# Kernel optimization log

Hardware: AMD Instinct MI355X
Metric: run time of the kernel (lower is better)

Reference implementation:

```python
import jax, jax.numpy as jnp
import numpy as np

N_LEAVES = 32768
DEPTH = 16               # tree levels, leaves at level 0
N_NODES = 2 * N_LEAVES - 1
H = 256                  # h_size
X = 300                  # x_size
FEAT = 1024              # image feature_size
R = 49                   # image regions
VOCAB = 30000
CLASSES = 5


def setup_inputs() -> dict:
    ks = jax.random.split(jax.random.key(0), 10)
    wordid = jax.random.randint(ks[0], (N_NODES,), 0, VOCAB, dtype=jnp.int32)
    # leaves carry word tokens (mask=1), internal nodes don't (mask=0)
    mask = jnp.concatenate([jnp.ones(N_LEAVES, jnp.int32),
                            jnp.zeros(N_NODES - N_LEAVES, jnp.int32)])
    image = jax.random.normal(ks[1], (R, FEAT), dtype=jnp.float32)
    h0 = jnp.zeros((N_NODES, H), jnp.float32)
    c0 = jnp.zeros((N_NODES, H), jnp.float32)
    s = lambda k, shp, fan: jax.random.normal(k, shp, dtype=jnp.float32) * (1.0 / np.sqrt(fan))
    emb = s(ks[2], (VOCAB, X), X)
    attn_w_in = s(ks[3], (X, FEAT), FEAT)            # Attention.linear_in (no bias)
    attn_w_out = s(ks[4], (X, X + FEAT), X + FEAT)   # Attention.linear_out
    attn_b_out = jnp.zeros((X,), jnp.float32)
    w_iou = s(ks[5], (3 * H, X), X)                  # cell.W_iou (no bias)
    u_iou = s(ks[6], (3 * H, 2 * H), 2 * H)          # cell.U_iou (no bias)
    b_iou = jnp.zeros((1, 3 * H), jnp.float32)
    u_f_w = s(ks[7], (2 * H, 2 * H), 2 * H)          # cell.U_f
    u_f_b = jnp.zeros((2 * H,), jnp.float32)
    lin_w = s(ks[8], (CLASSES, H), H)                # final classifier
    lin_b = jnp.zeros((CLASSES,), jnp.float32)
    return dict(wordid=wordid, mask=mask, image=image, h0=h0, c0=c0, emb=emb,
                attn_w_in=attn_w_in, attn_w_out=attn_w_out, attn_b_out=attn_b_out,
                w_iou=w_iou, u_iou=u_iou, b_iou=b_iou, u_f_w=u_f_w, u_f_b=u_f_b,
                lin_w=lin_w, lin_b=lin_b)


def _forward(wordid, mask, image, h0, c0, emb, attn_w_in, attn_w_out, attn_b_out,
             w_iou, u_iou, b_iou, u_f_w, u_f_b, lin_w, lin_b):
    # --- embedding + attention over image regions ---
    embeds = emb[wordid * mask]                                  # [N, X]
    img_in = image @ attn_w_in.T                                 # [R, X]
    atten = jax.nn.softmax(embeds @ img_in.T, axis=1)            # [N, R]
    context = atten @ image                                      # [N, FEAT]
    sent = jnp.tanh(jnp.concatenate([context, embeds], axis=1) @ attn_w_out.T + attn_b_out)
    iou_x = (sent @ w_iou.T) * mask[:, None].astype(sent.dtype)  # [N, 3H] (dropout p=0 -> identity)

    def apply_node(iou, c_in):
        i, o, u = jnp.split(iou + b_iou, 3, axis=1)
        c_new = jax.nn.sigmoid(i) * jnp.tanh(u) + c_in
        return jax.nn.sigmoid(o) * jnp.tanh(c_new), c_new

    # --- leaves: no mailbox, apply_node with initial c ---
    h_leaf, c_leaf = apply_node(iou_x[:N_LEAVES], c0[:N_LEAVES])
    h = h0.at[:N_LEAVES].set(h_leaf)
    c = c0.at[:N_LEAVES].set(c_leaf)

    # --- topological propagation, one dense level at a time ---
    off_prev, sz, off = 0, N_LEAVES, N_LEAVES
    for _ in range(DEPTH - 1):
        sz_new = sz // 2
        h_cat = jax.lax.dynamic_slice_in_dim(h, off_prev, sz).reshape(sz_new, 2 * H)
        c_ch = jax.lax.dynamic_slice_in_dim(c, off_prev, sz).reshape(sz_new, 2, H)
        f = jax.nn.sigmoid(h_cat @ u_f_w.T + u_f_b).reshape(sz_new, 2, H)
        c_red = jnp.sum(f * c_ch, axis=1)                        # [sz_new, H]
        iou = h_cat @ u_iou.T                                    # reduce_func overwrites node iou
        h_new, c_new = apply_node(iou, c_red)
        h = h.at[off:off + sz_new].set(h_new)
        c = c.at[off:off + sz_new].set(c_new)
        off_prev, sz, off = off, sz_new, off + sz_new

    return h @ lin_w.T + lin_b                                   # [N, CLASSES]


def reference(wordid, mask, image, h0, c0, emb, attn_w_in, attn_w_out, attn_b_out,
              w_iou, u_iou, b_iou, u_f_w, u_f_b, lin_w, lin_b):
    return _forward(wordid, mask, image, h0, c0, emb, attn_w_in, attn_w_out, attn_b_out,
                    w_iou, u_iou, b_iou, u_f_w, u_f_b, lin_w, lin_b)
```

## Files before the change

kernel.cpp:

```cpp
#include <hip/hip_runtime.h>
#include <hip/hip_bf16.h>
#include <math.h>

#define N_LEAVES 32768
#define N_NODES  65535
#define DEPTH    16
#define H        256
#define XS       300
#define FEAT     1024
#define RR       49
#define CLASSES  5

#define XP 320
#define CATW 384

typedef __attribute__((ext_vector_type(8))) short bf16x8;
typedef __attribute__((ext_vector_type(4))) float f32x4;

__device__ __forceinline__ ushort f2bf(float v) {
    __hip_bfloat16 h = __float2bfloat16(v);
    return *reinterpret_cast<ushort*>(&h);
}
__device__ __forceinline__ float bf2f(ushort u) {
    __hip_bfloat16 h; *reinterpret_cast<ushort*>(&h) = u;
    return __bfloat162float(h);
}

__device__ __forceinline__ float fsig(float x) {
    float e = __builtin_amdgcn_exp2f(-1.44269504f * x);
    return __builtin_amdgcn_rcpf(1.0f + e);
}
__device__ __forceinline__ float ftanh(float x) {
    float xx = fmaxf(x, -20.0f);
    float e = __builtin_amdgcn_exp2f(-2.88539008f * xx);
    return (1.0f - e) * __builtin_amdgcn_rcpf(1.0f + e);
}
__device__ __forceinline__ float fexp(float x) {
    return __builtin_amdgcn_exp2f(1.44269504f * x);
}

#define SPIN() __builtin_amdgcn_sched_barrier(0)
#define SBAR() { __builtin_amdgcn_s_barrier(); __builtin_amdgcn_sched_barrier(0); }

__device__ __forceinline__ void swz_mj(int& mblk, int& jg) {
    int lid = blockIdx.y * gridDim.x + blockIdx.x;
    int mcount = gridDim.y, njg = gridDim.x;
    if ((mcount & 7) == 0) {
        int xcd = lid & 7, q = lid >> 3;
        jg = q % njg;
        mblk = xcd * (mcount >> 3) + q / njg;
    } else { mblk = blockIdx.y; jg = blockIdx.x; }
}

__device__ __forceinline__ ushort* lds_at(ushort* base, int row, int kbyte) {
    int off = row * 128 + kbyte;
    off ^= ((row & 7) << 4);
    return (ushort*)((char*)base + off);
}

__device__ __forceinline__ void gll16(const void* g, void* l) {
    __builtin_amdgcn_global_load_lds(
        (const __attribute__((address_space(1))) unsigned int*)g,
        (__attribute__((address_space(3))) unsigned int*)l, 16, 0, 0);
}

__device__ __forceinline__ void issue_tileA(const ushort* A, long lda, long m0, long mmax,
                                            int k0, ushort* buf, int R, int w, int lane)
{
    const int insts = R >> 5;
#pragma unroll
    for (int q = 0; q < 4; ++q) {
        if (q >= insts) break;
        int dest = (w * insts + q) * 1024;
        int row = (dest >> 7) + (lane >> 3);
        int kb = ((lane & 7) << 4) ^ ((row & 7) << 4);
        long am = m0 + row; if (am > mmax) am = mmax;
        gll16((const char*)(A + am * lda + k0) + kb, (char*)buf + dest);
    }
}

__global__ __launch_bounds__(256)
void k_sent(const ushort* __restrict__ A, const ushort* __restrict__ Wf,
            const float* __restrict__ bias, ushort* __restrict__ Cbf)
{
    __shared__ ushort At[3][128 * 64];
    const int tid = threadIdx.x;
    const int l = tid & 63;
    const int w = tid >> 6;
    int mblk, nb; swz_mj(mblk, nb);
    const long m0 = (long)mblk * 128;
    const ushort* wb = Wf + (size_t)(nb * 4 + w) * 24 * 512 + l * 8;

    bf16x8 wreg[2][2][2];
    f32x4 acc[2][8] = {};

    auto loadW = [&](int t, int buf) {
        const ushort* wt = wb + (long)t * 4 * 512;
#pragma unroll
        for (int kk = 0; kk < 2; ++kk)
#pragma unroll
            for (int j = 0; j < 2; ++j)
                wreg[buf][kk][j] = *(const bf16x8*)(wt + (long)(kk * 2 + j) * 512);
    };

    issue_tileA(A, CATW, m0, N_LEAVES - 1, 0, At[0], 128, w, l);
    __syncthreads();
    issue_tileA(A, CATW, m0, N_LEAVES - 1, 64, At[1], 128, w, l);
    SPIN();
    loadW(0, 0);
#pragma unroll
    for (int t = 0; t < 6; ++t) {
        if (t + 2 < 6) issue_tileA(A, CATW, m0, N_LEAVES - 1, (t + 2) * 64, At[(t + 2) % 3], 128, w, l);
        SPIN();
        if (t + 1 < 6) loadW(t + 1, (t + 1) & 1);
        ushort* Ab = At[t % 3];
#pragma unroll
        for (int kk = 0; kk < 2; ++kk) {
            bf16x8 af[8];
#pragma unroll
            for (int i = 0; i < 8; ++i)
                af[i] = *(const bf16x8*)lds_at(Ab, i * 16 + (l & 15), kk * 64 + (l >> 4) * 16);
#pragma unroll
            for (int j = 0; j < 2; ++j)
#pragma unroll
                for (int i = 0; i < 8; ++i)
                    acc[j][i] = __builtin_amdgcn_mfma_f32_16x16x32_bf16(af[i], wreg[t & 1][kk][j], acc[j][i], 0, 0, 0);
        }
        if (t + 1 < 6) SBAR();
    }
#pragma unroll
    for (int j = 0; j < 2; ++j) {
        long n = (long)nb * 128 + w * 32 + j * 16 + (l & 15);
        if (n >= XS) continue;
        float bn = bias[n];
#pragma unroll
        for (int i = 0; i < 8; ++i)
#pragma unroll
            for (int r = 0; r < 4; ++r) {
                long m = m0 + i * 16 + (l >> 4) * 4 + r;
                Cbf[m * XP + n] = f2bf(ftanh(acc[j][i][r] + bn));
            }
    }
}

__global__ __launch_bounds__(256)
void k_attn(const float* __restrict__ emb, const int* __restrict__ wid,
            const ushort* __restrict__ img, ushort* __restrict__ cat)
{
    __shared__ ushort At[128 * 64];
    __shared__ ushort Bt[64 * 64];
    const int tid = threadIdx.x;
    const int l = tid & 63;
    const int w = tid >> 6;
    const long m0 = (long)blockIdx.x * 128;
    const int srow = tid >> 3, skg = tid & 7;

    int wrd[4];
#pragma unroll
    for (int q = 0; q < 4; ++q) wrd[q] = wid[m0 + q * 32 + srow];

    float av[4][8];
    bf16x8 breg[2];
    f32x4 acc[2][4] = {};

    auto loadAB = [&](int t) {
        int c = t * 64 + skg * 8;
#pragma unroll
        for (int q = 0; q < 4; ++q) {
            const float* er = emb + (long)wrd[q] * XS;
            if (c + 8 <= XS) {
                float4 a = *(const float4*)(er + c);
                float4 b = *(const float4*)(er + c + 4);
                av[q][0] = a.x; av[q][1] = a.y; av[q][2] = a.z; av[q][3] = a.w;
                av[q][4] = b.x; av[q][5] = b.y; av[q][6] = b.z; av[q][7] = b.w;
            } else {
#pragma unroll
                for (int u = 0; u < 8; ++u) av[q][u] = (c + u < XS) ? er[c + u] : 0.f;
            }
        }
#pragma unroll
        for (int q = 0; q < 2; ++q)
            breg[q] = *(const bf16x8*)(img + (long)(q * 32 + srow) * XP + t * 64 + skg * 8);
    };
    auto writeAB = [&](int t) {
        int c = t * 64 + skg * 8;
#pragma unroll
        for (int q = 0; q < 4; ++q) {
            int row = q * 32 + srow;
            bf16x8 pk;
#pragma unroll
            for (int u = 0; u < 8; ++u) pk[u] = (short)f2bf(av[q][u]);
            *(bf16x8*)lds_at(At, row, skg * 16) = pk;
            *(bf16x8*)(cat + (m0 + row) * CATW + 64 + c) = pk;
        }
#pragma unroll
        for (int q = 0; q < 2; ++q)
            *(bf16x8*)lds_at(Bt, q * 32 + srow, skg * 16) = breg[q];
    };

    loadAB(0);
    writeAB(0);
    for (int t = 0; t < 5; ++t) {
        __syncthreads();
        if (t + 1 < 5) loadAB(t + 1);
#pragma unroll
        for (int kk = 0; kk < 2; ++kk) {
            bf16x8 af[2], bg[4];
#pragma unroll
            for (int i = 0; i < 2; ++i)
                af[i] = *(const bf16x8*)lds_at(At, w * 32 + i * 16 + (l & 15), kk * 64 + (l >> 4) * 16);
#pragma unroll
            for (int j = 0; j < 4; ++j)
                bg[j] = *(const bf16x8*)lds_at(Bt, j * 16 + (l & 15), kk * 64 + (l >> 4) * 16);
#pragma unroll
            for (int i = 0; i < 2; ++i)
#pragma unroll
                for (int j = 0; j < 4; ++j)
                    acc[i][j] = __builtin_amdgcn_mfma_f32_16x16x32_bf16(af[i], bg[j], acc[i][j], 0, 0, 0);
        }
        if (t + 1 < 5) {
            __syncthreads();
            writeAB(t + 1);
        }
    }
#pragma unroll
    for (int i = 0; i < 2; ++i)
#pragma unroll
        for (int r = 0; r < 4; ++r) {
            long m = m0 + w * 32 + i * 16 + (l >> 4) * 4 + r;
            float v[4]; float mx = -1e30f;
#pragma unroll
            for (int j = 0; j < 4; ++j) {
                int n = j * 16 + (l & 15);
                v[j] = (n < RR) ? acc[i][j][r] : -1e30f;
                mx = fmaxf(mx, v[j]);
            }
#pragma unroll
            for (int sh = 1; sh < 16; sh <<= 1) mx = fmaxf(mx, __shfl_xor(mx, sh));
            float e[4], s = 0.f;
#pragma unroll
            for (int j = 0; j < 4; ++j) { e[j] = fexp(v[j] - mx); s += e[j]; }
#pragma unroll
            for (int sh = 1; sh < 16; sh <<= 1) s += __shfl_xor(s, sh);
            float inv = __builtin_amdgcn_rcpf(s);
#pragma unroll
            for (int j = 0; j < 4; ++j)
                cat[m * CATW + j * 16 + (l & 15)] = f2bf(e[j] * inv);
        }
}

__global__ __launch_bounds__(256)
void k_leaf_fused(const ushort* __restrict__ A, const ushort* __restrict__ Wf,
                  const float* __restrict__ b_iou,
                  ushort* __restrict__ h, ushort* __restrict__ c)
{
    __shared__ ushort At[3][128 * 64];
    const int tid = threadIdx.x;
    const int l = tid & 63;
    const int w = tid >> 6;
    int mblk, jg; swz_mj(mblk, jg);
    const long m0 = (long)mblk * 128;
    const ushort* wb = Wf + (size_t)(jg * 4 + w) * 30 * 512 + l * 8;

    bf16x8 wreg[2][2][3];
    f32x4 acc[3][8] = {};

    auto loadW = [&](int t, int buf) {
        const ushort* wt = wb + (long)t * 6 * 512;
#pragma unroll
        for (int kk = 0; kk < 2; ++kk)
#pragma unroll
            for (int g = 0; g < 3; ++g)
                wreg[buf][kk][g] = *(const bf16x8*)(wt + (long)(kk * 3 + g) * 512);
    };

    issue_tileA(A, XP, m0, N_LEAVES - 1, 0, At[0], 128, w, l);
    __syncthreads();
    issue_tileA(A, XP, m0, N_LEAVES - 1, 64, At[1], 128, w, l);
    SPIN();
    loadW(0, 0);
#pragma unroll
    for (int t = 0; t < 5; ++t) {
        if (t + 2 < 5) issue_tileA(A, XP, m0, N_LEAVES - 1, (t + 2) * 64, At[(t + 2) % 3], 128, w, l);
        SPIN();
        if (t + 1 < 5) loadW(t + 1, (t + 1) & 1);
        ushort* Ab = At[t % 3];
#pragma unroll
        for (int kk = 0; kk < 2; ++kk) {
            bf16x8 af[8];
#pragma unroll
            for (int i = 0; i < 8; ++i)
                af[i] = *(const bf16x8*)lds_at(Ab, i * 16 + (l & 15), kk * 64 + (l >> 4) * 16);
#pragma unroll
            for (int g = 0; g < 3; ++g)
#pragma unroll
                for (int i = 0; i < 8; ++i)
                    acc[g][i] = __builtin_amdgcn_mfma_f32_16x16x32_bf16(af[i], wreg[t & 1][kk][g], acc[g][i], 0, 0, 0);
        }
        if (t + 1 < 5) SBAR();
    }
    {
        int jglob = jg * 64 + w * 16 + (l & 15);
        float bi = b_iou[jglob], bu = b_iou[512 + jglob], bo = b_iou[256 + jglob];
#pragma unroll
        for (int i = 0; i < 8; ++i)
#pragma unroll
            for (int r = 0; r < 4; ++r) {
                long m = m0 + i * 16 + (l >> 4) * 4 + r;
                float cn = fsig(acc[0][i][r] + bi) * ftanh(acc[1][i][r] + bu);
                c[m * H + jglob] = f2bf(cn);
                h[m * H + jglob] = f2bf(fsig(acc[2][i][r] + bo) * ftanh(cn));
            }
    }
}

__global__ __launch_bounds__(256)
void k_tree_fused(const ushort* __restrict__ A, const ushort* __restrict__ Wf,
                  const float* __restrict__ u_f_b, const float* __restrict__ b_iou,
                  const ushort* __restrict__ csrc,
                  ushort* __restrict__ hdst, ushort* __restrict__ cdst, int sz_new)
{
    __shared__ ushort At[5][64 * 64];
    const int tid = threadIdx.x;
    const int l = tid & 63;
    const int w = tid >> 6;
    int mblk, jg; swz_mj(mblk, jg);
    const long m0 = (long)mblk * 64;
    const ushort* wb = Wf + (size_t)(jg * 4 + w) * 80 * 512 + l * 8;

    bf16x8 wreg[2][2][5];
    f32x4 acc[5][4] = {};

    auto loadW = [&](int t, int buf) {
        const ushort* wt = wb + (long)t * 10 * 512;
#pragma unroll
        for (int kk = 0; kk < 2; ++kk)
#pragma unroll
            for (int g = 0; g < 5; ++g)
                wreg[buf][kk][g] = *(const bf16x8*)(wt + (long)(kk * 5 + g) * 512);
    };

    issue_tileA(A, 512, m0, sz_new - 1, 0, At[0], 64, w, l);
    __syncthreads();
    issue_tileA(A, 512, m0, sz_new - 1, 64, At[1], 64, w, l);
    SPIN();
    loadW(0, 0);
    SPIN();
    issue_tileA(A, 512, m0, sz_new - 1, 128, At[2], 64, w, l);
    SPIN();
    issue_tileA(A, 512, m0, sz_new - 1, 192, At[3], 64, w, l);
#pragma unroll
    for (int t = 0; t < 8; ++t) {
        if (t + 1 < 8) loadW(t + 1, (t + 1) & 1);
        SPIN();
        if (t + 4 < 8) issue_tileA(A, 512, m0, sz_new - 1, (t + 4) * 64, At[(t + 4) % 5], 64, w, l);
        SPIN();
        ushort* Ab = At[t % 5];
#pragma unroll
        for (int kk = 0; kk < 2; ++kk) {
            bf16x8 af[4];
#pragma unroll
            for (int i = 0; i < 4; ++i)
                af[i] = *(const bf16x8*)lds_at(Ab, i * 16 + (l & 15), kk * 64 + (l >> 4) * 16);
#pragma unroll
            for (int g = 0; g < 5; ++g)
#pragma unroll
                for (int i = 0; i < 4; ++i)
                    acc[g][i] = __builtin_amdgcn_mfma_f32_16x16x32_bf16(af[i], wreg[t & 1][kk][g], acc[g][i], 0, 0, 0);
        }
        if (t + 1 < 8) SBAR();
    }
    {
        int jglob = jg * 64 + w * 16 + (l & 15);
        float bf0 = u_f_b[jglob], bf1 = u_f_b[256 + jglob];
        float bi = b_iou[jglob], bu = b_iou[512 + jglob], bo = b_iou[256 + jglob];
#pragma unroll
        for (int i = 0; i < 4; ++i)
#pragma unroll
            for (int r = 0; r < 4; ++r) {
                long m = m0 + i * 16 + (l >> 4) * 4 + r;
                if (m < sz_new) {
                    float cl = bf2f(csrc[(2 * m) * H + jglob]);
                    float cr = bf2f(csrc[(2 * m + 1) * H + jglob]);
                    float S = fsig(acc[0][i][r] + bf0) * cl
                            + fsig(acc[1][i][r] + bf1) * cr;
                    float cn = fsig(acc[2][i][r] + bi) * ftanh(acc[3][i][r] + bu) + S;
                    cdst[m * H + jglob] = f2bf(cn);
                    hdst[m * H + jglob] = f2bf(fsig(acc[4][i][r] + bo) * ftanh(cn));
                }
            }
    }
}

__global__ __launch_bounds__(256)
void k_tree_small(const ushort* __restrict__ A, const ushort* __restrict__ Wf,
                  const float* __restrict__ u_f_b, const float* __restrict__ b_iou,
                  const ushort* __restrict__ csrc,
                  ushort* __restrict__ hdst, ushort* __restrict__ cdst, int sz_new)
{
    __shared__ ushort At[5][64 * 64];
    const int tid = threadIdx.x;
    const int l = tid & 63;
    const int w = tid >> 6;
    const int mblk = blockIdx.y, jg = blockIdx.x;
    const long m0 = (long)mblk * 64;
    const ushort* wb = Wf + (size_t)(jg * 4 + w) * 80 * 512 + l * 8;

    bf16x8 wreg[3][2][5];
    f32x4 acc[5][4] = {};

    auto loadW = [&](int t, int buf) {
        const ushort* wt = wb + (long)t * 10 * 512;
#pragma unroll
        for (int kk = 0; kk < 2; ++kk)
#pragma unroll
            for (int g = 0; g < 5; ++g)
                wreg[buf][kk][g] = *(const bf16x8*)(wt + (long)(kk * 5 + g) * 512);
    };

    issue_tileA(A, 512, m0, sz_new - 1, 0, At[0], 64, w, l);
    __syncthreads();
    issue_tileA(A, 512, m0, sz_new - 1, 64, At[1], 64, w, l);
    SPIN();
    loadW(0, 0);
    SPIN();
    loadW(1, 1);
    SPIN();
    issue_tileA(A, 512, m0, sz_new - 1, 128, At[2], 64, w, l);
    SPIN();
    issue_tileA(A, 512, m0, sz_new - 1, 192, At[3], 64, w, l);
#pragma unroll
    for (int t = 0; t < 8; ++t) {
        if (t + 2 < 8) loadW(t + 2, (t + 2) % 3);
        SPIN();
        if (t + 4 < 8) issue_tileA(A, 512, m0, sz_new - 1, (t + 4) * 64, At[(t + 4) % 5], 64, w, l);
        SPIN();
        ushort* Ab = At[t % 5];
#pragma unroll
        for (int kk = 0; kk < 2; ++kk) {
            bf16x8 af[4];
#pragma unroll
            for (int i = 0; i < 4; ++i)
                af[i] = *(const bf16x8*)lds_at(Ab, i * 16 + (l & 15), kk * 64 + (l >> 4) * 16);
#pragma unroll
            for (int g = 0; g < 5; ++g)
#pragma unroll
                for (int i = 0; i < 4; ++i)
                    acc[g][i] = __builtin_amdgcn_mfma_f32_16x16x32_bf16(af[i], wreg[t % 3][kk][g], acc[g][i], 0, 0, 0);
        }
        if (t + 1 < 8) SBAR();
    }
    {
        int jglob = jg * 64 + w * 16 + (l & 15);
        float bf0 = u_f_b[jglob], bf1 = u_f_b[256 + jglob];
        float bi = b_iou[jglob], bu = b_iou[512 + jglob], bo = b_iou[256 + jglob];
#pragma unroll
        for (int i = 0; i < 4; ++i)
#pragma unroll
            for (int r = 0; r < 4; ++r) {
                long m = m0 + i * 16 + (l >> 4) * 4 + r;
                if (m < sz_new) {
                    float cl = bf2f(csrc[(2 * m) * H + jglob]);
                    float cr = bf2f(csrc[(2 * m + 1) * H + jglob]);
                    float S = fsig(acc[0][i][r] + bf0) * cl
                            + fsig(acc[1][i][r] + bf1) * cr;
                    float cn = fsig(acc[2][i][r] + bi) * ftanh(acc[3][i][r] + bu) + S;
                    cdst[m * H + jglob] = f2bf(cn);
                    hdst[m * H + jglob] = f2bf(fsig(acc[4][i][r] + bo) * ftanh(cn));
                }
            }
    }
}

#define PREP_NB   7350
#define CVT_NB    352
#define W3F_NB    960
#define W5F_NB    2560

__global__ __launch_bounds__(256)
void k_prep_a(const float* __restrict__ image, const float* __restrict__ w_in,
              const float* __restrict__ w_out, const float* __restrict__ w_iou,
              const float* __restrict__ u_f_w, const float* __restrict__ u_iou,
              ushort* __restrict__ img_bf, ushort* __restrict__ wcat,
              ushort* __restrict__ w3f, ushort* __restrict__ w5f)
{
    int b = blockIdx.x;
    if (b < PREP_NB) {
        const int wave = (b * 256 + threadIdx.x) >> 6;
        const int lane = threadIdx.x & 63;
        const int half = RR * XS;
        if (wave >= 2 * half) return;
        const float* wr; const float* ir; ushort* outp;
        if (wave < half) {
            int r = wave / XS, x = wave % XS;
            ir = image + (long)r * FEAT;
            wr = w_in + (long)x * FEAT;
            outp = img_bf + (long)r * XP + x;
        } else {
            int w2 = wave - half;
            int x = w2 / RR, r = w2 % RR;
            ir = image + (long)r * FEAT;
            wr = w_out + (long)x * (FEAT + XS);
            outp = wcat + (long)x * CATW + r;
        }
        float s = 0.f;
#pragma unroll
        for (int u = 0; u < FEAT / 64; ++u) {
            int f = lane + u * 64;
            s = fmaf(ir[f], wr[f], s);
        }
#pragma unroll
        for (int sh = 32; sh; sh >>= 1) s += __shfl_xor(s, sh);
        if (lane == 0) *outp = f2bf(s);
    } else if (b < PREP_NB + CVT_NB) {
        long idx = (long)(b - PREP_NB) * 256 + threadIdx.x;
        if (idx >= (long)XS * XS) return;
        int r = (int)(idx / XS), cc = (int)(idx % XS);
        wcat[(long)r * CATW + 64 + cc] = f2bf(w_out[(long)r * (FEAT + XS) + FEAT + cc]);
    } else if (b < PREP_NB + CVT_NB + W3F_NB) {
        long idx = (long)(b - PREP_NB - CVT_NB) * 256 + threadIdx.x;
        if (idx >= 245760) return;
        int u = idx & 7; long r = idx >> 3;
        int l = r & 63; r >>= 6;
        int g = (int)(r % 3); r /= 3;
        int kk = r & 1; r >>= 1;
        int t = (int)(r % 5); r /= 5;
        int wq = r & 3; r >>= 2;
        int jg = (int)r;
        int row = jg * 64 + wq * 16 + (l & 15);
        int col = t * 64 + kk * 32 + (l >> 4) * 8 + u;
        int srow = (g == 0) ? row : (g == 1) ? 512 + row : 256 + row;
        w3f[idx] = (col < XS) ? f2bf(w_iou[(long)srow * XS + col]) : 0;
    } else {
        long idx = (long)(b - PREP_NB - CVT_NB - W3F_NB) * 256 + threadIdx.x;
        if (idx >= 655360) return;
        int u = idx & 7; long r = idx >> 3;
        int l = r & 63; r >>= 6;
        int g = (int)(r % 5); r /= 5;
        int kk = r & 1; r >>= 1;
        int t = (int)(r & 7); r >>= 3;
        int wq = r & 3; r >>= 2;
        int jg = (int)r;
        int row = jg * 64 + wq * 16 + (l & 15);
        int col = t * 64 + kk * 32 + (l >> 4) * 8 + u;
        const float* src;
        if (g == 0)      src = u_f_w + (long)row * 512;
        else if (g == 1) src = u_f_w + (long)(256 + row) * 512;
        else if (g == 2) src = u_iou + (long)row * 512;
        else if (g == 3) src = u_iou + (long)(512 + row) * 512;
        else             src = u_iou + (long)(256 + row) * 512;
        w5f[idx] = f2bf(src[col]);
    }
}

__global__ __launch_bounds__(256)
void k_prep_b(ushort* __restrict__ dst, const ushort* __restrict__ wcat)
{
    long idx = (long)blockIdx.x * 256 + threadIdx.x;
    if (idx >= 147456) return;
    int u = idx & 7; long r = idx >> 3;
    int l = r & 63; r >>= 6;
    int j = r & 1; r >>= 1;
    int kk = r & 1; r >>= 1;
    int t = (int)(r % 6); r /= 6;
    int wq = r & 3; r >>= 2;
    int nb = (int)r;
    int row = nb * 128 + wq * 32 + j * 16 + (l & 15);
    int col = t * 64 + kk * 32 + (l >> 4) * 8 + u;
    dst[idx] = wcat[(long)row * CATW + col];
}

__global__ __launch_bounds__(256)
void k_classify(const ushort* __restrict__ h, const float* __restrict__ lin_w,
                const float* __restrict__ lin_b, float* __restrict__ out, int n_rows)
{
    const long t = (long)blockIdx.x * 256 + threadIdx.x;
    const int node = (int)(t >> 4);
    const int li = (int)(t & 15);
    if (node >= n_rows) return;
    const ushort* hr = h + (long)node * H + li * 16;
    bf16x8 h0 = *(const bf16x8*)(hr);
    bf16x8 h1 = *(const bf16x8*)(hr + 8);
    float hv[16];
#pragma unroll
    for (int u = 0; u < 8; ++u) {
        hv[u] = bf2f((ushort)h0[u]);
        hv[8 + u] = bf2f((ushort)h1[u]);
    }
    float p[CLASSES];
#pragma unroll
    for (int cc = 0; cc < CLASSES; ++cc) {
        const float* wr = lin_w + (long)cc * H + li * 16;
        float4 w0 = *(const float4*)(wr);
        float4 w1 = *(const float4*)(wr + 4);
        float4 w2 = *(const float4*)(wr + 8);
        float4 w3 = *(const float4*)(wr + 12);
        float s = hv[0] * w0.x + hv[1] * w0.y + hv[2] * w0.z + hv[3] * w0.w;
        s = fmaf(hv[4], w1.x, s); s = fmaf(hv[5], w1.y, s);
        s = fmaf(hv[6], w1.z, s); s = fmaf(hv[7], w1.w, s);
        s = fmaf(hv[8], w2.x, s); s = fmaf(hv[9], w2.y, s);
        s = fmaf(hv[10], w2.z, s); s = fmaf(hv[11], w2.w, s);
        s = fmaf(hv[12], w3.x, s); s = fmaf(hv[13], w3.y, s);
        s = fmaf(hv[14], w3.z, s); s = fmaf(hv[15], w3.w, s);
        p[cc] = s;
    }
#pragma unroll
    for (int cc = 0; cc < CLASSES; ++cc)
#pragma unroll
        for (int sh = 1; sh < 16; sh <<= 1) p[cc] += __shfl_xor(p[cc], sh);
    if (li == 0) {
#pragma unroll
        for (int cc = 0; cc < CLASSES; ++cc)
            out[(long)node * CLASSES + cc] = p[cc] + lin_b[cc];
    }
}

extern "C" void kernel_launch(void* const* d_in, const int* in_sizes, int n_in,
                              void* d_out, int out_size, void* d_ws, size_t ws_size,
                              hipStream_t stream)
{
    const int*   wordid     = (const int*)  d_in[0];
    const float* image      = (const float*)d_in[2];
    const float* emb        = (const float*)d_in[5];
    const float* attn_w_in  = (const float*)d_in[6];
    const float* attn_w_out = (const float*)d_in[7];
    const float* attn_b_out = (const float*)d_in[8];
    const float* w_iou      = (const float*)d_in[9];
    const float* u_iou      = (const float*)d_in[10];
    const float* b_iou      = (const float*)d_in[11];
    const float* u_f_w      = (const float*)d_in[12];
    const float* u_f_b      = (const float*)d_in[13];
    const float* lin_w      = (const float*)d_in[14];
    const float* lin_b      = (const float*)d_in[15];
    float* out = (float*)d_out;

    char* p = (char*)d_ws;
    auto alloc = [&](size_t bytes) { char* r = p; p += (bytes + 255) & ~255UL; return r; };
    ushort* cat     = (ushort*)alloc((size_t)N_LEAVES * CATW * 2);
    ushort* sentbf  = (ushort*)alloc((size_t)N_LEAVES * XP * 2);
    ushort* hall    = (ushort*)alloc((size_t)65536 * H * 2);
    ushort* cA      = (ushort*)alloc((size_t)N_LEAVES * H * 2);
    ushort* cB      = (ushort*)alloc((size_t)(N_LEAVES/2) * H * 2);
    ushort* img_bf  = (ushort*)alloc((size_t)64 * XP * 2);
    ushort* wcat    = (ushort*)alloc((size_t)CATW * CATW * 2);
    ushort* wcatf   = (ushort*)alloc((size_t)147456 * 2);
    ushort* w3f     = (ushort*)alloc((size_t)245760 * 2);
    ushort* w5f     = (ushort*)alloc((size_t)655360 * 2);
    (void)ws_size;

    hipMemsetAsync(img_bf, 0, (size_t)64 * XP * 2 + (size_t)CATW * CATW * 2, stream);
    k_prep_a<<<PREP_NB + CVT_NB + W3F_NB + W5F_NB, 256, 0, stream>>>(
        image, attn_w_in, attn_w_out, w_iou, u_f_w, u_iou,
        img_bf, wcat, w3f, w5f);
    k_prep_b<<<(147456 + 255) / 256, 256, 0, stream>>>(wcatf, wcat);

    k_attn<<<N_LEAVES / 128, 256, 0, stream>>>(emb, wordid, img_bf, cat);
    k_sent<<<dim3(3, N_LEAVES / 128), 256, 0, stream>>>(cat, wcatf, attn_b_out, sentbf);
    k_leaf_fused<<<dim3(4, N_LEAVES / 128), 256, 0, stream>>>(
        sentbf, w3f, b_iou, hall, cA);

    ushort* csrc = cA; ushort* cdst = cB;
    int node_off = N_LEAVES;
    int sz = N_LEAVES;
    int off_prev = 0;
    for (int lvl = 0; lvl < DEPTH - 1; ++lvl) {
        int sz_new = sz / 2;
        dim3 g(4, (sz_new + 63) / 64);
        if (sz_new > 256)
            k_tree_fused<<<g, 256, 0, stream>>>(
                hall + (long)off_prev * H, w5f, u_f_b, b_iou, csrc,
                hall + (long)node_off * H, cdst, sz_new);
        else
            k_tree_small<<<g, 256, 0, stream>>>(
                hall + (long)off_prev * H, w5f, u_f_b, b_iou, csrc,
                hall + (long)node_off * H, cdst, sz_new);
        off_prev = node_off;
        node_off += sz_new;
        ushort* t = csrc; csrc = cdst; cdst = t;
        sz = sz_new;
    }

    k_classify<<<(int)(((long)N_NODES * 16 + 255) / 256), 256, 0, stream>>>(
        hall, lin_w, lin_b, out, N_NODES);
}
```

Baseline: 302.1 us.

## Restructure attention kernel: single-shot embedding staging and pre-swizzled image fragments

The attention-score kernel now processes 64 rows per block instead of 128 and stages the whole embedding tile into LDS in one pass, replacing the old double-buffered K loop and its repeated barriers. The image matrix is pre-swizzled into MFMA fragment order by an extra branch in the prep kernel, so each wave reads B operands straight from global memory (cached) instead of through LDS. This gives more blocks and fewer synchronisations for a small kernel, at the cost of more global loads of the small image matrix and larger LDS per block.

```diff
diff --git a/kernel.cpp b/kernel.cpp
--- a/kernel.cpp
+++ b/kernel.cpp
@@ -145,94 +145,62 @@
 
 __global__ __launch_bounds__(256)
 void k_attn(const float* __restrict__ emb, const int* __restrict__ wid,
-            const ushort* __restrict__ img, ushort* __restrict__ cat)
-{
-    __shared__ ushort At[128 * 64];
-    __shared__ ushort Bt[64 * 64];
+            const ushort* __restrict__ imgf, ushort* __restrict__ cat)
+{
+    __shared__ ushort E[5][64 * 64];
     const int tid = threadIdx.x;
     const int l = tid & 63;
     const int w = tid >> 6;
-    const long m0 = (long)blockIdx.x * 128;
-    const int srow = tid >> 3, skg = tid & 7;
-
-    int wrd[4];
-#pragma unroll
-    for (int q = 0; q < 4; ++q) wrd[q] = wid[m0 + q * 32 + srow];
-
-    float av[4][8];
-    bf16x8 breg[2];
-    f32x4 acc[2][4] = {};
-
-    auto loadAB = [&](int t) {
-        int c = t * 64 + skg * 8;
-#pragma unroll
-        for (int q = 0; q < 4; ++q) {
-            const float* er = emb + (long)wrd[q] * XS;
-            if (c + 8 <= XS) {
-                float4 a = *(const float4*)(er + c);
-                float4 b = *(const float4*)(er + c + 4);
-                av[q][0] = a.x; av[q][1] = a.y; av[q][2] = a.z; av[q][3] = a.w;
-                av[q][4] = b.x; av[q][5] = b.y; av[q][6] = b.z; av[q][7] = b.w;
+    const long m0 = (long)blockIdx.x * 64;
+
+    {
+        int row = tid >> 2;
+        int q = tid & 3;
+        const float* er = emb + (long)wid[m0 + row] * XS;
+#pragma unroll
+        for (int u = 0; u < 10; ++u) {
+            int ccol = q * 80 + u * 8;
+            bf16x8 pk;
+            if (ccol + 8 <= XS) {
+                float4 a = *(const float4*)(er + ccol);
+                float4 b = *(const float4*)(er + ccol + 4);
+                pk[0] = (short)f2bf(a.x); pk[1] = (short)f2bf(a.y);
+                pk[2] = (short)f2bf(a.z); pk[3] = (short)f2bf(a.w);
+                pk[4] = (short)f2bf(b.x); pk[5] = (short)f2bf(b.y);
+                pk[6] = (short)f2bf(b.z); pk[7] = (short)f2bf(b.w);
             } else {
 #pragma unroll
-                for (int u = 0; u < 8; ++u) av[q][u] = (c + u < XS) ? er[c + u] : 0.f;
+                for (int e = 0; e < 8; ++e)
+                    pk[e] = (ccol + e < XS) ? (short)f2bf(er[ccol + e]) : (short)0;
             }
-        }
-#pragma unroll
-        for (int q = 0; q < 2; ++q)
-            breg[q] = *(const bf16x8*)(img + (long)(q * 32 + srow) * XP + t * 64 + skg * 8);
-    };
-    auto writeAB = [&](int t) {
-        int c = t * 64 + skg * 8;
-#pragma unroll
-        for (int q = 0; q < 4; ++q) {
-            int row = q * 32 + srow;
-            bf16x8 pk;
-#pragma unroll
-            for (int u = 0; u < 8; ++u) pk[u] = (short)f2bf(av[q][u]);
-            *(bf16x8*)lds_at(At, row, skg * 16) = pk;
-            *(bf16x8*)(cat + (m0 + row) * CATW + 64 + c) = pk;
-        }
-#pragma unroll
-        for (int q = 0; q < 2; ++q)
-            *(bf16x8*)lds_at(Bt, q * 32 + srow, skg * 16) = breg[q];
-    };
-
-    loadAB(0);
-    writeAB(0);
-    for (int t = 0; t < 5; ++t) {
-        __syncthreads();
-        if (t + 1 < 5) loadAB(t + 1);
-#pragma unroll
-        for (int kk = 0; kk < 2; ++kk) {
-            bf16x8 af[2], bg[4];
-#pragma unroll
-            for (int i = 0; i < 2; ++i)
-                af[i] = *(const bf16x8*)lds_at(At, w * 32 + i * 16 + (l & 15), kk * 64 + (l >> 4) * 16);
-#pragma unroll
-            for (int j = 0; j < 4; ++j)
-                bg[j] = *(const bf16x8*)lds_at(Bt, j * 16 + (l & 15), kk * 64 + (l >> 4) * 16);
-#pragma unroll
-            for (int i = 0; i < 2; ++i)
-#pragma unroll
-                for (int j = 0; j < 4; ++j)
-                    acc[i][j] = __builtin_amdgcn_mfma_f32_16x16x32_bf16(af[i], bg[j], acc[i][j], 0, 0, 0);
-        }
-        if (t + 1 < 5) {
-            __syncthreads();
-            writeAB(t + 1);
-        }
-    }
-#pragma unroll
-    for (int i = 0; i < 2; ++i)
+            *(bf16x8*)lds_at(E[ccol >> 6], row, (ccol & 63) * 2) = pk;
+            *(bf16x8*)(cat + (m0 + row) * CATW + 64 + ccol) = pk;
+        }
+    }
+    __syncthreads();
+
+    {
+        f32x4 sacc[4] = {};
+        const ushort* ib = imgf + l * 8;
+#pragma unroll
+        for (int t = 0; t < 5; ++t)
+#pragma unroll
+            for (int kk = 0; kk < 2; ++kk) {
+                bf16x8 af = *(const bf16x8*)lds_at(E[t], w * 16 + (l & 15), kk * 64 + (l >> 4) * 16);
+#pragma unroll
+                for (int j = 0; j < 4; ++j) {
+                    bf16x8 bg = *(const bf16x8*)(ib + (long)((j * 5 + t) * 2 + kk) * 512);
+                    sacc[j] = __builtin_amdgcn_mfma_f32_16x16x32_bf16(af, bg, sacc[j], 0, 0, 0);
+                }
+            }
 #pragma unroll
         for (int r = 0; r < 4; ++r) {
-            long m = m0 + w * 32 + i * 16 + (l >> 4) * 4 + r;
+            int row = w * 16 + (l >> 4) * 4 + r;
             float v[4]; float mx = -1e30f;
 #pragma unroll
             for (int j = 0; j < 4; ++j) {
                 int n = j * 16 + (l & 15);
-                v[j] = (n < RR) ? acc[i][j][r] : -1e30f;
+                v[j] = (n < RR) ? sacc[j][r] : -1e30f;
                 mx = fmaxf(mx, v[j]);
             }
 #pragma unroll
@@ -245,8 +213,9 @@
             float inv = __builtin_amdgcn_rcpf(s);
 #pragma unroll
             for (int j = 0; j < 4; ++j)
-                cat[m * CATW + j * 16 + (l & 15)] = f2bf(e[j] * inv);
-        }
+                cat[(m0 + row) * CATW + j * 16 + (l & 15)] = f2bf(e[j] * inv);
+        }
+    }
 }
 
 __global__ __launch_bounds__(256)
@@ -553,21 +522,38 @@
     }
 }
 
-__global__ __launch_bounds__(256)
-void k_prep_b(ushort* __restrict__ dst, const ushort* __restrict__ wcat)
-{
-    long idx = (long)blockIdx.x * 256 + threadIdx.x;
-    if (idx >= 147456) return;
-    int u = idx & 7; long r = idx >> 3;
-    int l = r & 63; r >>= 6;
-    int j = r & 1; r >>= 1;
-    int kk = r & 1; r >>= 1;
-    int t = (int)(r % 6); r /= 6;
-    int wq = r & 3; r >>= 2;
-    int nb = (int)r;
-    int row = nb * 128 + wq * 32 + j * 16 + (l & 15);
-    int col = t * 64 + kk * 32 + (l >> 4) * 8 + u;
-    dst[idx] = wcat[(long)row * CATW + col];
+#define WCATF_NB 576
+#define IMGF_NB  80
+__global__ __launch_bounds__(256)
+void k_prep_b(ushort* __restrict__ wcatf, ushort* __restrict__ imgf,
+              const ushort* __restrict__ wcat, const ushort* __restrict__ img_bf)
+{
+    int b = blockIdx.x;
+    if (b < WCATF_NB) {
+        long idx = (long)b * 256 + threadIdx.x;
+        if (idx >= 147456) return;
+        int u = idx & 7; long r = idx >> 3;
+        int l = r & 63; r >>= 6;
+        int j = r & 1; r >>= 1;
+        int kk = r & 1; r >>= 1;
+        int t = (int)(r % 6); r /= 6;
+        int wq = r & 3; r >>= 2;
+        int nb = (int)r;
+        int row = nb * 128 + wq * 32 + j * 16 + (l & 15);
+        int col = t * 64 + kk * 32 + (l >> 4) * 8 + u;
+        wcatf[idx] = wcat[(long)row * CATW + col];
+    } else {
+        long idx = (long)(b - WCATF_NB) * 256 + threadIdx.x;
+        if (idx >= 20480) return;
+        int u = idx & 7; long r = idx >> 3;
+        int l = r & 63; r >>= 6;
+        int kk = r & 1; r >>= 1;
+        int t = (int)(r % 5); r /= 5;
+        int j = (int)r;
+        int row = j * 16 + (l & 15);
+        int col = t * 64 + kk * 32 + (l >> 4) * 8 + u;
+        imgf[idx] = img_bf[(long)row * XP + col];
+    }
 }
 
 __global__ __launch_bounds__(256)
@@ -643,6 +629,7 @@
     ushort* cB      = (ushort*)alloc((size_t)(N_LEAVES/2) * H * 2);
     ushort* img_bf  = (ushort*)alloc((size_t)64 * XP * 2);
     ushort* wcat    = (ushort*)alloc((size_t)CATW * CATW * 2);
+    ushort* imgf    = (ushort*)alloc((size_t)20480 * 2);
     ushort* wcatf   = (ushort*)alloc((size_t)147456 * 2);
     ushort* w3f     = (ushort*)alloc((size_t)245760 * 2);
     ushort* w5f     = (ushort*)alloc((size_t)655360 * 2);
@@ -652,9 +639,9 @@
     k_prep_a<<<PREP_NB + CVT_NB + W3F_NB + W5F_NB, 256, 0, stream>>>(
         image, attn_w_in, attn_w_out, w_iou, u_f_w, u_iou,
         img_bf, wcat, w3f, w5f);
-    k_prep_b<<<(147456 + 255) / 256, 256, 0, stream>>>(wcatf, wcat);
-
-    k_attn<<<N_LEAVES / 128, 256, 0, stream>>>(emb, wordid, img_bf, cat);
+    k_prep_b<<<WCATF_NB + IMGF_NB, 256, 0, stream>>>(wcatf, imgf, wcat, img_bf);
+
+    k_attn<<<N_LEAVES / 64, 256, 0, stream>>>(emb, wordid, imgf, cat);
     k_sent<<<dim3(3, N_LEAVES / 128), 256, 0, stream>>>(cat, wcatf, attn_b_out, sentbf);
     k_leaf_fused<<<dim3(4, N_LEAVES / 128), 256, 0, stream>>>(
         sentbf, w3f, b_iou, hall, cA);
```

Result: slower. 313.2 us (+3.7%).
